# Performance work log

Measured on AMD Instinct MI355X. Metric: run time of the kernel, lower is better.

## Reference

```python
import jax, jax.numpy as jnp
import numpy as np

SIGNAL = (32, 32)
KERNEL = (8, 8)
N_FEATURES = [64, 128, 128]
BATCH = 64
ALPHA = 0.5          # source references an undefined global `alpha`; fixed here
LEAKY_SLOPE = 0.01   # torch F.leaky_relu default


def _join_tensor(S, K, loc):
    i = np.arange(S)[:, None, None]
    j = np.arange(S)[None, :, None]
    k = np.arange(K)[None, None, :]
    M = (j >= i) & (i == np.maximum(j, k + loc))
    return jnp.asarray(M.astype(np.float32))


def _meet_tensor(S, K, loc):
    i = np.arange(S)[:, None, None]
    j = np.arange(S)[None, :, None]
    k = np.arange(K)[None, None, :]
    M = (j >= i) & (i == np.minimum(j, k + loc))
    return jnp.asarray(M.astype(np.float32))


def setup_inputs() -> dict:
    key = jax.random.key(0)
    sx, sy = SIGNAL
    kx, ky = KERNEL
    # meet layers use kernel_loc = signal - kernel; join layers use (0, 0)
    cmx = _meet_tensor(sx, kx, sx - kx)
    cmy = _meet_tensor(sy, ky, sy - ky)
    cjx = _join_tensor(sx, kx, 0)
    cjy = _join_tensor(sy, ky, 0)

    keys = jax.random.split(key, 16)
    x = jax.random.normal(keys[0], (BATCH, N_FEATURES[0], sx, sy), dtype=jnp.float32)

    def kaiming(k, shape):
        fan_in = shape[0] * shape[1] * shape[2]  # kx*ky*in_features
        return jax.random.normal(k, shape, dtype=jnp.float32) * np.float32(np.sqrt(2.0 / fan_in))

    inp = {"x": x, "cmx": cmx, "cmy": cmy, "cjx": cjx, "cjy": cjy}
    for li in range(len(N_FEATURES) - 1):
        fi, fo = N_FEATURES[li], N_FEATURES[li + 1]
        inp[f"mw{li}"] = kaiming(keys[1 + 2 * li], (kx, ky, fi, fo))
        inp[f"mb{li}"] = jnp.zeros((fo, 1, 1), dtype=jnp.float32)
        inp[f"jw{li}"] = kaiming(keys[2 + 2 * li], (kx, ky, fi, fo))
        inp[f"jb{li}"] = jnp.zeros((fo, 1, 1), dtype=jnp.float32)
    return inp


def _lattice_conv(cx, cy, X, W, b):
    # Y[m,g,x,y] = sum_{i,j,a,b} cx[i,x,a] cy[j,y,b] X[m,f,i,j] W[a,b,f,g] + bias
    return jnp.einsum('ixa,jyb,mfij,abfg->mgxy', cx, cy, X, W, optimize='optimal') + b


def reference(x, cmx, cmy, cjx, cjy, mw0, mb0, jw0, jb0, mw1, mb1, jw1, jb1):
    params = [(mw0, mb0, jw0, jb0), (mw1, mb1, jw1, jb1)]
    for mw, mb, jw, jb in params:
        m = _lattice_conv(cmx, cmy, x, mw, mb)
        j = _lattice_conv(cjx, cjy, x, jw, jb)
        x = jax.nn.leaky_relu((1.0 - ALPHA) * m + ALPHA * j, negative_slope=LEAKY_SLOPE)
    return x
```

## Files before the change

### kernel.cpp

```cpp
#include <hip/hip_runtime.h>
#include <stdint.h>


typedef __attribute__((ext_vector_type(8))) short short8;
typedef __attribute__((ext_vector_type(4))) float floatx4;

__device__ __forceinline__ float bf2f(unsigned short u) {
  union { uint32_t u; float f; } c; c.u = ((uint32_t)u) << 16; return c.f;
}
__device__ __forceinline__ unsigned short f2bf(float f) {
  union { float f; uint32_t u; } c; c.f = f;
  uint32_t u = c.u;
  uint32_t r = (u + 0x7FFFu + ((u >> 16) & 1u)) >> 16;
  return (unsigned short)r;
}

__global__ void detect_and_bias(const unsigned short* __restrict__ xa,
                                const void* __restrict__ mb0,
                                const void* __restrict__ jb0,
                                const void* __restrict__ mb1,
                                const void* __restrict__ jb1,
                                float* __restrict__ bias0,
                                float* __restrict__ bias1,
                                int* __restrict__ flag) {
  __shared__ int cnt;
  if (threadIdx.x == 0) cnt = 0;
  __syncthreads();
  unsigned short v = xa[threadIdx.x];
  int e = (v >> 7) & 0xFF;
  int ok = (v == 0) || (e >= 110 && e <= 140);
  atomicAdd(&cnt, ok);
  __syncthreads();
  int fp32 = (cnt >= 240) ? 0 : 1;
  if (threadIdx.x == 0) *flag = fp32;
  int g = threadIdx.x & 127;
  const void* mb = (threadIdx.x < 128) ? mb0 : mb1;
  const void* jb = (threadIdx.x < 128) ? jb0 : jb1;
  float* bo = (threadIdx.x < 128) ? bias0 : bias1;
  float m = fp32 ? ((const float*)mb)[g] : bf2f(((const unsigned short*)mb)[g]);
  float j = fp32 ? ((const float*)jb)[g] : bf2f(((const unsigned short*)jb)[g]);
  bo[g] = 0.5f * (m + j);
}

__global__ __launch_bounds__(256) void transpose_in(
    const unsigned short* __restrict__ s16, const float* __restrict__ s32,
    unsigned short* __restrict__ dst, int R, int C,
    const int* __restrict__ flag) {
  __shared__ unsigned short tile[32][33];
  int fp32 = *flag;
  int tx = threadIdx.x, ty = threadIdx.y;
  int c0 = blockIdx.x * 32, r0 = blockIdx.y * 32;
  if (fp32) {
#pragma unroll
    for (int i = 0; i < 32; i += 8)
      tile[ty + i][tx] = f2bf(s32[(size_t)(r0 + ty + i) * C + (c0 + tx)]);
  } else {
#pragma unroll
    for (int i = 0; i < 32; i += 8)
      tile[ty + i][tx] = s16[(size_t)(r0 + ty + i) * C + (c0 + tx)];
  }
  __syncthreads();
#pragma unroll
  for (int i = 0; i < 32; i += 8)
    dst[(size_t)(c0 + ty + i) * R + (r0 + tx)] = tile[tx][ty + i];
}

__global__ __launch_bounds__(256) void transpose_out(
    const unsigned short* __restrict__ src, unsigned short* __restrict__ d16,
    float* __restrict__ d32, int R, int C, const int* __restrict__ flag) {
  __shared__ unsigned short tile[32][33];
  int fp32 = *flag;
  int tx = threadIdx.x, ty = threadIdx.y;
  int c0 = blockIdx.x * 32, r0 = blockIdx.y * 32;
#pragma unroll
  for (int i = 0; i < 32; i += 8)
    tile[ty + i][tx] = src[(size_t)(r0 + ty + i) * C + (c0 + tx)];
  __syncthreads();
  if (fp32) {
#pragma unroll
    for (int i = 0; i < 32; i += 8)
      d32[(size_t)(c0 + ty + i) * R + (r0 + tx)] = bf2f(tile[tx][ty + i]);
  } else {
#pragma unroll
    for (int i = 0; i < 32; i += 8)
      d16[(size_t)(c0 + ty + i) * R + (r0 + tx)] = tile[tx][ty + i];
  }
}

#define SLOT_W1 0
#define SLOT_SB 225
#define SLOT_AS 289
#define SLOT_M  353
#define N_SLOTS 417

__global__ __launch_bounds__(256) void prep_stageA(
    const void* __restrict__ mw0, const void* __restrict__ jw0,
    const void* __restrict__ mw1, const void* __restrict__ jw1,
    unsigned short* __restrict__ Int0, unsigned short* __restrict__ Int1,
    const int* __restrict__ flag) {
  int layer = blockIdx.z;
  int FG = layer ? 16384 : 8192;
  int fg = blockIdx.x * 256 + threadIdx.x;
  if (fg >= FG) return;
  int fp32 = *flag;
  const void* mw = layer ? mw1 : mw0;
  unsigned short* Int = layer ? Int1 : Int0;
  int group = blockIdx.y;

  float w[64];
#pragma unroll
  for (int ab = 0; ab < 64; ++ab) {
    size_t idx = (size_t)ab * FG + fg;
    w[ab] = fp32 ? ((const float*)mw)[idx]
                 : bf2f(((const unsigned short*)mw)[idx]);
  }
  if (group == 3) {
#pragma unroll
    for (int ab = 0; ab < 64; ++ab)
      Int[(size_t)(SLOT_M + ab) * FG + fg] = f2bf(0.5f * w[ab]);
    return;
  }
#pragma unroll
  for (int a = 0; a < 8; ++a)
#pragma unroll
    for (int b = 6; b >= 0; --b) w[a * 8 + b] += w[a * 8 + b + 1];
  if (group == 2) {
#pragma unroll
    for (int ab = 0; ab < 64; ++ab)
      Int[(size_t)(SLOT_AS + ab) * FG + fg] = f2bf(0.5f * w[ab]);
  }
#pragma unroll
  for (int a = 6; a >= 0; --a)
#pragma unroll
    for (int b = 0; b < 8; ++b) w[a * 8 + b] += w[(a + 1) * 8 + b];
  if (group == 2) {
#pragma unroll
    for (int px = 0; px < 8; ++px)
#pragma unroll
      for (int b = 0; b < 8; ++b) {
        float v = w[px * 8 + b] - (b < 7 ? w[px * 8 + b + 1] : 0.0f);
        Int[(size_t)(SLOT_SB + px * 8 + b) * FG + fg] = f2bf(0.5f * v);
      }
    return;
  }
  const void* jw = layer ? jw1 : jw0;
  float pp[64];
#pragma unroll
  for (int ab = 0; ab < 64; ++ab) {
    size_t idx = (size_t)ab * FG + fg;
    pp[ab] = fp32 ? ((const float*)jw)[idx]
                  : bf2f(((const unsigned short*)jw)[idx]);
  }
#pragma unroll
  for (int a = 0; a < 8; ++a)
#pragma unroll
    for (int b = 1; b < 8; ++b) pp[a * 8 + b] += pp[a * 8 + b - 1];
#pragma unroll
  for (int a = 1; a < 8; ++a)
#pragma unroll
    for (int b = 0; b < 8; ++b) pp[a * 8 + b] += pp[(a - 1) * 8 + b];
  int cx0 = (group == 0) ? 0 : 7, cx1 = (group == 0) ? 7 : 15;
  for (int cx = cx0; cx < cx1; ++cx) {
    int pmx = cx < 7 ? cx : 7;
    int pxx = cx > 7 ? cx - 7 : 0;
#pragma unroll
    for (int cy = 0; cy < 15; ++cy) {
      int pmy = cy < 7 ? cy : 7;
      int pyy = cy > 7 ? cy - 7 : 0;
      float v = 0.5f * (w[pxx * 8 + pyy] + pp[pmx * 8 + pmy]);
      Int[(size_t)(SLOT_W1 + cx * 15 + cy) * FG + fg] = f2bf(v);
    }
  }
}

__global__ __launch_bounds__(256) void prep_stageB(
    const unsigned short* __restrict__ Int0,
    const unsigned short* __restrict__ Int1,
    unsigned short* __restrict__ Wall0, unsigned short* __restrict__ Wall1) {
  int zz = blockIdx.z;
  int layer = (zz >= N_SLOTS) ? 1 : 0;
  int slot = zz - layer * N_SLOTS;
  int F = layer ? 128 : 64;
  int f0 = blockIdx.y * 32;
  if (f0 >= F) return;
  int g0 = blockIdx.x * 32;
  const unsigned short* src =
      (layer ? Int1 : Int0) + (size_t)slot * F * 128;
  unsigned short* dst = (layer ? Wall1 : Wall0) + (size_t)slot * F * 128;
  __shared__ unsigned short tile[32][33];
  int tx = threadIdx.x, ty = threadIdx.y;
#pragma unroll
  for (int i = 0; i < 32; i += 8)
    tile[ty + i][tx] = src[(size_t)(f0 + ty + i) * 128 + (g0 + tx)];
  __syncthreads();
#pragma unroll
  for (int i = 0; i < 32; i += 8)
    dst[(size_t)(g0 + ty + i) * F + (f0 + tx)] = tile[tx][ty + i];
}

template <int F, int NT>
__device__ __forceinline__ void mfma_tile(
    const unsigned short* __restrict__ A, const unsigned short* __restrict__ W,
    floatx4 acc[NT], int wave, int n, int q) {
  const unsigned short* a_ptr = A + ((size_t)(wave * 16 + n)) * F + q * 8;
  const unsigned short* w_ptr = W + (size_t)n * F + q * 8;
#pragma unroll
  for (int kk = 0; kk < F; kk += 32) {
    short8 av = *(const short8*)(a_ptr + kk);
#pragma unroll
    for (int t = 0; t < NT; ++t) {
      short8 bv = *(const short8*)(w_ptr + (size_t)t * 16 * F + kk);
      acc[t] = __builtin_amdgcn_mfma_f32_16x16x32_bf16(av, bv, acc[t], 0, 0, 0);
    }
  }
}

template <int F>
__global__ __launch_bounds__(256) void corr_gemm(
    const unsigned short* __restrict__ Xt, const unsigned short* __restrict__ Wall,
    float* __restrict__ V, float* __restrict__ U, float* __restrict__ T) {
  int bid = blockIdx.x, gs = blockIdx.y;
  int wave = threadIdx.x >> 6, lane = threadIdx.x & 63;
  int n = lane & 15, q = lane >> 4;
  int ipos, slot;
  float* out;
  if (bid < 256) {
    int a = bid >> 5, y = bid & 31;
    int py = y > 24 ? y - 24 : 0;
    ipos = (24 + a) * 32 + y;
    slot = SLOT_AS + a * 8 + py;
    out = V + (size_t)(a * 32 + y) * 8192;
  } else if (bid < 512) {
    int i = bid - 256;
    int b = i >> 5, x = i & 31;
    int px = x > 24 ? x - 24 : 0;
    ipos = x * 32 + 24 + b;
    slot = SLOT_SB + px * 8 + b;
    out = U + (size_t)(b * 32 + x) * 8192;
  } else {
    int i = bid - 512;
    int a = i >> 3, b = i & 7;
    ipos = (24 + a) * 32 + 24 + b;
    slot = SLOT_M + a * 8 + b;
    out = T + (size_t)(a * 8 + b) * 8192;
  }
  floatx4 acc[4];
#pragma unroll
  for (int t = 0; t < 4; ++t) acc[t] = (floatx4){0.f, 0.f, 0.f, 0.f};
  mfma_tile<F, 4>(Xt + (size_t)ipos * 64 * F,
                  Wall + ((size_t)slot * 128 + gs * 64) * F, acc, wave, n, q);
#pragma unroll
  for (int t = 0; t < 4; ++t) {
    int gcol = gs * 64 + t * 16 + n;
#pragma unroll
    for (int r = 0; r < 4; ++r) {
      int m = wave * 16 + q * 4 + r;
      out[(size_t)m * 128 + gcol] = acc[t][r];
    }
  }
}

__global__ __launch_bounds__(256) void scan_corr(float* __restrict__ V,
                                                 float* __restrict__ U,
                                                 float* __restrict__ T) {
  int b = blockIdx.x;
  if (b < 2048) {
    float* base = (b < 1024) ? V : U;
    int tid = ((b & 1023) * 256 + threadIdx.x);
    float* p = base + (size_t)tid;
    float s = 0.f;
#pragma unroll
    for (int a = 0; a < 8; ++a) {
      s += p[(size_t)a * 262144];
      p[(size_t)a * 262144] = s;
    }
  } else {
    int mg = (b - 2048) * 256 + threadIdx.x;
    float col[8];
#pragma unroll
    for (int i = 0; i < 8; ++i) col[i] = 0.f;
#pragma unroll
    for (int a = 0; a < 8; ++a) {
      float rs = 0.f;
#pragma unroll
      for (int bb = 0; bb < 8; ++bb) {
        size_t idx = (size_t)(a * 8 + bb) * 8192 + mg;
        col[bb] += T[idx];
        rs += col[bb];
        T[idx] = rs;
      }
    }
  }
}

template <int F>
__global__ __launch_bounds__(256) void final_gemm(
    const unsigned short* __restrict__ Xt, const unsigned short* __restrict__ Wall,
    const float* __restrict__ V, const float* __restrict__ U,
    const float* __restrict__ T, const float* __restrict__ bias,
    unsigned short* __restrict__ Out) {
  int pos = blockIdx.x, gs = blockIdx.y;
  int x = pos >> 5, y = pos & 31;
  int wave = threadIdx.x >> 6, lane = threadIdx.x & 63;
  int n = lane & 15, q = lane >> 4;
  int clsx = x < 7 ? x : (x <= 24 ? 7 : x - 17);
  int clsy = y < 7 ? y : (y <= 24 ? 7 : y - 17);
  int px = x > 24 ? x - 24 : 0;
  int py = y > 24 ? y - 24 : 0;
  const float* c3 = px ? V + ((size_t)(px - 1) * 32 + y) * 8192 : nullptr;
  const float* c2 = py ? U + ((size_t)(py - 1) * 32 + x) * 8192 : nullptr;
  const float* c4 =
      (px && py) ? T + (size_t)((px - 1) * 8 + (py - 1)) * 8192 : nullptr;

  float csum[4][4];
#pragma unroll
  for (int t = 0; t < 4; ++t) {
    int gcol = gs * 64 + t * 16 + n;
    float bv = bias[gcol];
#pragma unroll
    for (int r = 0; r < 4; ++r) {
      int m = wave * 16 + q * 4 + r;
      size_t idx = (size_t)m * 128 + gcol;
      float v = bv;
      if (c3) v += c3[idx];
      if (c2) v += c2[idx];
      if (c4) v += c4[idx];
      csum[t][r] = v;
    }
  }

  floatx4 acc[4];
#pragma unroll
  for (int t = 0; t < 4; ++t) acc[t] = (floatx4){0.f, 0.f, 0.f, 0.f};
  mfma_tile<F, 4>(Xt + (size_t)pos * 64 * F,
                  Wall + ((size_t)(SLOT_W1 + clsx * 15 + clsy) * 128 + gs * 64) * F,
                  acc, wave, n, q);

  unsigned short* o = Out + (size_t)pos * 64 * 128;
#pragma unroll
  for (int t = 0; t < 4; ++t) {
    int gcol = gs * 64 + t * 16 + n;
#pragma unroll
    for (int r = 0; r < 4; ++r) {
      int m = wave * 16 + q * 4 + r;
      float v = acc[t][r] + csum[t][r];
      v = v > 0.f ? v : 0.01f * v;
      o[(size_t)m * 128 + gcol] = f2bf(v);
    }
  }
}

extern "C" void kernel_launch(void* const* d_in, const int* in_sizes, int n_in,
                              void* d_out, int out_size, void* d_ws,
                              size_t ws_size, hipStream_t stream) {
  const void* x   = d_in[0];
  const void* mw0 = d_in[5];
  const void* mb0 = d_in[6];
  const void* jw0 = d_in[7];
  const void* jb0 = d_in[8];
  const void* mw1 = d_in[9];
  const void* mb1 = d_in[10];
  const void* jw1 = d_in[11];
  const void* jb1 = d_in[12];

  char* ws = (char*)d_ws;
  const size_t MB = 1u << 20;
  unsigned short* Xt0   = (unsigned short*)(ws + 0);
  unsigned short* A1    = (unsigned short*)(ws + 9 * MB);
  unsigned short* Wall0 = (unsigned short*)(ws + 26 * MB);
  unsigned short* Wall1 = (unsigned short*)(ws + 33 * MB);
  unsigned short* Int0  = (unsigned short*)(ws + 47 * MB);
  unsigned short* Int1  = (unsigned short*)(ws + 54 * MB);
  unsigned short* Out2  = (unsigned short*)(ws + 68 * MB);
  float* bias0 = (float*)(ws + 85 * MB);
  float* bias1 = bias0 + 128;
  int*   flag  = (int*)(bias1 + 128);
  float* V = (float*)d_out;
  float* U = V + (size_t)8 * 32 * 8192;
  float* T = U + (size_t)8 * 32 * 8192;

  dim3 tb(32, 8);
  detect_and_bias<<<1, 256, 0, stream>>>((const unsigned short*)x, mb0, jb0,
                                         mb1, jb1, bias0, bias1, flag);
  prep_stageA<<<dim3(64, 4, 2), 256, 0, stream>>>(mw0, jw0, mw1, jw1, Int0,
                                                  Int1, flag);
  prep_stageB<<<dim3(4, 4, 2 * N_SLOTS), tb, 0, stream>>>(Int0, Int1, Wall0,
                                                          Wall1);
  transpose_in<<<dim3(32, 128), tb, 0, stream>>>(
      (const unsigned short*)x, (const float*)x, Xt0, 4096, 1024, flag);

  corr_gemm<64><<<dim3(576, 2), 256, 0, stream>>>(Xt0, Wall0, V, U, T);
  scan_corr<<<2080, 256, 0, stream>>>(V, U, T);
  final_gemm<64><<<dim3(1024, 2), 256, 0, stream>>>(Xt0, Wall0, V, U, T,
                                                    bias0, A1);
  corr_gemm<128><<<dim3(576, 2), 256, 0, stream>>>(A1, Wall1, V, U, T);
  scan_corr<<<2080, 256, 0, stream>>>(V, U, T);
  final_gemm<128><<<dim3(1024, 2), 256, 0, stream>>>(A1, Wall1, V, U, T,
                                                     bias1, Out2);

  transpose_out<<<dim3(256, 32), tb, 0, stream>>>(
      Out2, (unsigned short*)d_out, (float*)d_out, 1024, 8192, flag);
}
```

Measured before the change: 290.2 us.

## Recast weight prefix-sum preprocessing as an MFMA GEMM with a constant selection matrix

Replaces the per-thread scalar prefix-sum weight preparation with three steps. Weights are packed into a K=128 bf16 layout, a constant 0/0.5 selection matrix L (448x128) is built, and Int is computed as L times the packed weights using bf16 MFMA. This targets the register-heavy scalar kernel, which holds 128 floats per thread and makes strided global loads. In exchange it adds two extra launches and rounds the weights to bf16 before the summation, which changes numerics slightly.

```diff
diff --git a/kernel.cpp b/kernel.cpp
--- a/kernel.cpp
+++ b/kernel.cpp
@@ -92,83 +92,102 @@
 #define SLOT_AS 289
 #define SLOT_M  353
 #define N_SLOTS 417
-
-__global__ __launch_bounds__(256) void prep_stageA(
+#define N_SLOTS_PAD 448
+
+__global__ __launch_bounds__(256) void pack_weights(
     const void* __restrict__ mw0, const void* __restrict__ jw0,
     const void* __restrict__ mw1, const void* __restrict__ jw1,
-    unsigned short* __restrict__ Int0, unsigned short* __restrict__ Int1,
+    unsigned short* __restrict__ PB0, unsigned short* __restrict__ PB1,
     const int* __restrict__ flag) {
   int layer = blockIdx.z;
   int FG = layer ? 16384 : 8192;
-  int fg = blockIdx.x * 256 + threadIdx.x;
-  if (fg >= FG) return;
+  int c0 = blockIdx.x * 32;
+  if (c0 >= FG) return;
+  int kt = blockIdx.y;
+  const void* src = (kt < 2) ? (layer ? mw1 : mw0) : (layer ? jw1 : jw0);
+  unsigned short* PB = layer ? PB1 : PB0;
+  int r0 = (kt & 1) * 32;
   int fp32 = *flag;
-  const void* mw = layer ? mw1 : mw0;
+  __shared__ unsigned short tile[32][33];
+  int tx = threadIdx.x, ty = threadIdx.y;
+#pragma unroll
+  for (int i = 0; i < 32; i += 8) {
+    size_t idx = (size_t)(r0 + ty + i) * FG + (c0 + tx);
+    tile[ty + i][tx] = fp32 ? f2bf(((const float*)src)[idx])
+                            : ((const unsigned short*)src)[idx];
+  }
+  __syncthreads();
+#pragma unroll
+  for (int i = 0; i < 32; i += 8)
+    PB[(size_t)(c0 + ty + i) * 128 + (kt * 32 + tx)] = tile[tx][ty + i];
+}
+
+__global__ __launch_bounds__(256) void build_L(unsigned short* __restrict__ L) {
+  int tid = blockIdx.x * 256 + threadIdx.x;
+  int slot = tid >> 7, k = tid & 127;
+  int isj = k >= 64, ab = k & 63, a = ab >> 3, b = ab & 7;
+  float v = 0.f;
+  if (slot < 225) {
+    int cx = slot / 15, cy = slot % 15;
+    int pmx = cx < 7 ? cx : 7, pxx = cx > 7 ? cx - 7 : 0;
+    int pmy = cy < 7 ? cy : 7, pyy = cy > 7 ? cy - 7 : 0;
+    if (!isj) v = (a >= pxx && b >= pyy) ? 0.5f : 0.f;
+    else      v = (a <= pmx && b <= pmy) ? 0.5f : 0.f;
+  } else if (slot < 289) {
+    int s = slot - SLOT_SB, px = s >> 3, b0 = s & 7;
+    if (!isj) v = (a >= px && b == b0) ? 0.5f : 0.f;
+  } else if (slot < 353) {
+    int s = slot - SLOT_AS, a0 = s >> 3, py = s & 7;
+    if (!isj) v = (a == a0 && b >= py) ? 0.5f : 0.f;
+  } else if (slot < 417) {
+    int s = slot - SLOT_M, a0 = s >> 3, b0 = s & 7;
+    if (!isj) v = (a == a0 && b == b0) ? 0.5f : 0.f;
+  }
+  L[tid] = f2bf(v);
+}
+
+template <int F, int NT>
+__device__ __forceinline__ void mfma_tile(
+    const unsigned short* __restrict__ A, const unsigned short* __restrict__ W,
+    floatx4 acc[NT], int wave, int n, int q) {
+  const unsigned short* a_ptr = A + ((size_t)(wave * 16 + n)) * F + q * 8;
+  const unsigned short* w_ptr = W + (size_t)n * F + q * 8;
+#pragma unroll
+  for (int kk = 0; kk < F; kk += 32) {
+    short8 av = *(const short8*)(a_ptr + kk);
+#pragma unroll
+    for (int t = 0; t < NT; ++t) {
+      short8 bv = *(const short8*)(w_ptr + (size_t)t * 16 * F + kk);
+      acc[t] = __builtin_amdgcn_mfma_f32_16x16x32_bf16(av, bv, acc[t], 0, 0, 0);
+    }
+  }
+}
+
+__global__ __launch_bounds__(256) void prep_gemm(
+    const unsigned short* __restrict__ L,
+    const unsigned short* __restrict__ PB0,
+    const unsigned short* __restrict__ PB1,
+    unsigned short* __restrict__ Int0, unsigned short* __restrict__ Int1) {
+  int layer = blockIdx.z;
+  int FG = layer ? 16384 : 8192;
+  int n0 = blockIdx.x * 128;
+  if (n0 >= FG) return;
+  int m0 = blockIdx.y * 64;
+  const unsigned short* PB = layer ? PB1 : PB0;
   unsigned short* Int = layer ? Int1 : Int0;
-  int group = blockIdx.y;
-
-  float w[64];
-#pragma unroll
-  for (int ab = 0; ab < 64; ++ab) {
-    size_t idx = (size_t)ab * FG + fg;
-    w[ab] = fp32 ? ((const float*)mw)[idx]
-                 : bf2f(((const unsigned short*)mw)[idx]);
-  }
-  if (group == 3) {
-#pragma unroll
-    for (int ab = 0; ab < 64; ++ab)
-      Int[(size_t)(SLOT_M + ab) * FG + fg] = f2bf(0.5f * w[ab]);
-    return;
-  }
-#pragma unroll
-  for (int a = 0; a < 8; ++a)
-#pragma unroll
-    for (int b = 6; b >= 0; --b) w[a * 8 + b] += w[a * 8 + b + 1];
-  if (group == 2) {
-#pragma unroll
-    for (int ab = 0; ab < 64; ++ab)
-      Int[(size_t)(SLOT_AS + ab) * FG + fg] = f2bf(0.5f * w[ab]);
-  }
-#pragma unroll
-  for (int a = 6; a >= 0; --a)
-#pragma unroll
-    for (int b = 0; b < 8; ++b) w[a * 8 + b] += w[(a + 1) * 8 + b];
-  if (group == 2) {
-#pragma unroll
-    for (int px = 0; px < 8; ++px)
-#pragma unroll
-      for (int b = 0; b < 8; ++b) {
-        float v = w[px * 8 + b] - (b < 7 ? w[px * 8 + b + 1] : 0.0f);
-        Int[(size_t)(SLOT_SB + px * 8 + b) * FG + fg] = f2bf(0.5f * v);
-      }
-    return;
-  }
-  const void* jw = layer ? jw1 : jw0;
-  float pp[64];
-#pragma unroll
-  for (int ab = 0; ab < 64; ++ab) {
-    size_t idx = (size_t)ab * FG + fg;
-    pp[ab] = fp32 ? ((const float*)jw)[idx]
-                  : bf2f(((const unsigned short*)jw)[idx]);
-  }
-#pragma unroll
-  for (int a = 0; a < 8; ++a)
-#pragma unroll
-    for (int b = 1; b < 8; ++b) pp[a * 8 + b] += pp[a * 8 + b - 1];
-#pragma unroll
-  for (int a = 1; a < 8; ++a)
-#pragma unroll
-    for (int b = 0; b < 8; ++b) pp[a * 8 + b] += pp[(a - 1) * 8 + b];
-  int cx0 = (group == 0) ? 0 : 7, cx1 = (group == 0) ? 7 : 15;
-  for (int cx = cx0; cx < cx1; ++cx) {
-    int pmx = cx < 7 ? cx : 7;
-    int pxx = cx > 7 ? cx - 7 : 0;
-#pragma unroll
-    for (int cy = 0; cy < 15; ++cy) {
-      int pmy = cy < 7 ? cy : 7;
-      int pyy = cy > 7 ? cy - 7 : 0;
-      float v = 0.5f * (w[pxx * 8 + pyy] + pp[pmx * 8 + pmy]);
-      Int[(size_t)(SLOT_W1 + cx * 15 + cy) * FG + fg] = f2bf(v);
+  int wave = threadIdx.x >> 6, lane = threadIdx.x & 63;
+  int n = lane & 15, q = lane >> 4;
+  floatx4 acc[8];
+#pragma unroll
+  for (int t = 0; t < 8; ++t) acc[t] = (floatx4){0.f, 0.f, 0.f, 0.f};
+  mfma_tile<128, 8>(L + (size_t)m0 * 128, PB + (size_t)n0 * 128, acc, wave, n, q);
+#pragma unroll
+  for (int t = 0; t < 8; ++t) {
+    int gcol = n0 + t * 16 + n;
+#pragma unroll
+    for (int r = 0; r < 4; ++r) {
+      int m = m0 + wave * 16 + q * 4 + r;
+      Int[(size_t)m * FG + gcol] = f2bf(acc[t][r]);
     }
   }
 }
@@ -196,23 +215,6 @@
 #pragma unroll
   for (int i = 0; i < 32; i += 8)
     dst[(size_t)(g0 + ty + i) * F + (f0 + tx)] = tile[tx][ty + i];
-}
-
-template <int F, int NT>
-__device__ __forceinline__ void mfma_tile(
-    const unsigned short* __restrict__ A, const unsigned short* __restrict__ W,
-    floatx4 acc[NT], int wave, int n, int q) {
-  const unsigned short* a_ptr = A + ((size_t)(wave * 16 + n)) * F + q * 8;
-  const unsigned short* w_ptr = W + (size_t)n * F + q * 8;
-#pragma unroll
-  for (int kk = 0; kk < F; kk += 32) {
-    short8 av = *(const short8*)(a_ptr + kk);
-#pragma unroll
-    for (int t = 0; t < NT; ++t) {
-      short8 bv = *(const short8*)(w_ptr + (size_t)t * 16 * F + kk);
-      acc[t] = __builtin_amdgcn_mfma_f32_16x16x32_bf16(av, bv, acc[t], 0, 0, 0);
-    }
-  }
 }
 
 template <int F>
@@ -370,11 +372,14 @@
   unsigned short* Wall0 = (unsigned short*)(ws + 26 * MB);
   unsigned short* Wall1 = (unsigned short*)(ws + 33 * MB);
   unsigned short* Int0  = (unsigned short*)(ws + 47 * MB);
-  unsigned short* Int1  = (unsigned short*)(ws + 54 * MB);
-  unsigned short* Out2  = (unsigned short*)(ws + 68 * MB);
-  float* bias0 = (float*)(ws + 85 * MB);
+  unsigned short* Int1  = (unsigned short*)(ws + 55 * MB);
+  unsigned short* Out2  = (unsigned short*)(ws + 70 * MB);
+  float* bias0 = (float*)(ws + 87 * MB);
   float* bias1 = bias0 + 128;
   int*   flag  = (int*)(bias1 + 128);
+  unsigned short* PB0 = (unsigned short*)(ws + 88 * MB);
+  unsigned short* PB1 = (unsigned short*)(ws + 91 * MB);
+  unsigned short* L   = (unsigned short*)(ws + 96 * MB);
   float* V = (float*)d_out;
   float* U = V + (size_t)8 * 32 * 8192;
   float* T = U + (size_t)8 * 32 * 8192;
@@ -382,8 +387,10 @@
   dim3 tb(32, 8);
   detect_and_bias<<<1, 256, 0, stream>>>((const unsigned short*)x, mb0, jb0,
                                          mb1, jb1, bias0, bias1, flag);
-  prep_stageA<<<dim3(64, 4, 2), 256, 0, stream>>>(mw0, jw0, mw1, jw1, Int0,
-                                                  Int1, flag);
+  build_L<<<N_SLOTS_PAD * 128 / 256, 256, 0, stream>>>(L);
+  pack_weights<<<dim3(512, 4, 2), tb, 0, stream>>>(mw0, jw0, mw1, jw1, PB0,
+                                                   PB1, flag);
+  prep_gemm<<<dim3(128, 7, 2), 256, 0, stream>>>(L, PB0, PB1, Int0, Int1);
   prep_stageB<<<dim3(4, 4, 2 * N_SLOTS), tb, 0, stream>>>(Int0, Int1, Wall0,
                                                           Wall1);
   transpose_in<<<dim3(32, 128), tb, 0, stream>>>(
```

After: 272.2 us. -6.2%, faster.
